# Optimization experiments

Hardware: AMD Instinct MI355X
Metric: run time of the kernel (lower is better)

## Reference

```python
import jax, jax.numpy as jnp
import numpy as np

B, N, D, C = 8, 400, 768, 3
K = 0.4
# Original keeps ranked positions whose argsort value (original index) < k*N.
# That count is static: M = #{j in [0,N) : j < k*N}
M = int(np.sum(np.arange(N) < K * N))  # 160
# static off-diagonal pair index lists (i != j), row-major like the nested loops
_ii, _jj = np.nonzero(~np.eye(M, dtype=bool))
II = jnp.asarray(_ii)
JJ = jnp.asarray(_jj)


def setup_inputs() -> dict:
    key = jax.random.key(0)
    k1, k2, k3, k4 = jax.random.split(key, 4)
    x = jax.random.normal(k1, (B, N, D), dtype=jnp.float32)
    w_span = jax.random.normal(k2, (D, 1), dtype=jnp.float32) * 0.02
    b_span = jnp.zeros((1,), dtype=jnp.float32)
    w_pair = jax.random.normal(k3, (3 * D, C), dtype=jnp.float32) * 0.02
    b_pair = jnp.zeros((C,), dtype=jnp.float32)
    span_ranges = jax.random.randint(k4, (N, 2), 0, 40, dtype=jnp.int32)
    return {"x": x, "w_span": w_span, "b_span": b_span,
            "w_pair": w_pair, "b_pair": b_pair, "span_ranges": span_ranges}


def reference(x, w_span, b_span, w_pair, b_pair, span_ranges):
    # span scorer: Linear(D,1) + sigmoid -> [B, N]
    h = jax.nn.sigmoid(x @ w_span + b_span)[..., 0]
    # torch.argsort(descending=True)
    order = jnp.argsort(-h, axis=-1)  # [B, N], original span indices in rank order
    # keep ranked positions j where order[b, j] < k*N (exactly M per row)
    pos = jnp.sort(jnp.where(order < K * N, jnp.arange(N), N), axis=-1)[:, :M]  # [B, M]
    # gather selected spans (built under no_grad in the original)
    x_ranked = jax.lax.stop_gradient(jnp.take_along_axis(x, pos[:, :, None], axis=1))  # [B, M, D]
    ranges_ranked = span_ranges[pos]  # [B, M, 2]

    # pair scorer decomposed over the concat [x_i, x_j, x_i*x_j]
    w1, w2, w3 = w_pair[:D], w_pair[D:2 * D], w_pair[2 * D:]
    a = x_ranked @ w1  # [B, M, C] contribution of x_i
    b = x_ranked @ w2  # [B, M, C] contribution of x_j
    mult = x_ranked[:, :, None, :] * x_ranked[:, None, :, :]  # [B, M, M, D]
    logits = a[:, :, None, :] + b[:, None, :, :] + mult @ w3 + b_pair  # [B, M, M, C]
    probs = jax.nn.softmax(jax.nn.sigmoid(logits), axis=-1)

    pair_probs = probs[:, II, JJ]  # [B, M*(M-1), C], off-diagonal pairs
    pair_ranges = jnp.stack([ranges_ranked[:, II], ranges_ranked[:, JJ]], axis=2)  # [B, P, 2, 2]
    return pair_probs, pair_ranges
```

## Files before the change

kernel.cpp:

```cpp
#include <hip/hip_runtime.h>
#include <math.h>

constexpr int B_ = 8;
constexpr int N_ = 400;
constexpr int D_ = 768;
constexpr int M_ = 160;
constexpr int PAIRS_ = M_ * (M_ - 1);
constexpr size_t BMD_ = (size_t)B_ * M_ * D_;

typedef __attribute__((ext_vector_type(8))) short short8;
typedef __attribute__((ext_vector_type(4))) float floatx4;


__device__ __forceinline__ short f2bf(float f) {
  unsigned u = __float_as_uint(f);
  return (short)((u + 0x7fffu + ((u >> 16) & 1u)) >> 16);
}

__global__ __launch_bounds__(256) void k_span(const float* __restrict__ x,
                                              const float* __restrict__ w_span,
                                              double* __restrict__ z) {
  int row = blockIdx.x * 4 + (threadIdx.x >> 6);
  int lane = threadIdx.x & 63;
  const float* xr = x + (size_t)row * D_;
  double acc = 0.0;
#pragma unroll
  for (int it = 0; it < 3; ++it) {
    int d = it * 256 + lane * 4;
    float4 xv = *(const float4*)(xr + d);
    float4 wv = *(const float4*)(w_span + d);
    acc += (double)xv.x * wv.x + (double)xv.y * wv.y +
           (double)xv.z * wv.z + (double)xv.w * wv.w;
  }
#pragma unroll
  for (int off = 32; off > 0; off >>= 1)
    acc += __shfl_down(acc, off, 64);
  if (lane == 0) z[row] = acc;
}

__global__ __launch_bounds__(256) void k_rank(const double* __restrict__ z,
                                              int* __restrict__ pos) {
  __shared__ double zsh[N_];
  __shared__ int ranksh[M_];
  int b = blockIdx.x;
  int t = threadIdx.x;
  for (int j = t; j < N_; j += 256) zsh[j] = z[b * N_ + j];
  __syncthreads();
  if (t < M_) {
    double zi = zsh[t];
    int cnt = 0;
    for (int j = 0; j < N_; ++j) {
      double zj = zsh[j];
      cnt += (zj > zi) || (zj == zi && j < t);
    }
    ranksh[t] = cnt;
  }
  __syncthreads();
  if (t < M_) {
    int r = ranksh[t];
    int slot = 0;
#pragma unroll 8
    for (int k = 0; k < M_; ++k) slot += (ranksh[k] < r);
    pos[b * M_ + slot] = r;
  }
}

__global__ __launch_bounds__(256) void k_prep_ranked(const float* __restrict__ x,
                                                     const float* __restrict__ w_pair,
                                                     const float* __restrict__ b_pair,
                                                     const int* __restrict__ pos,
                                                     const int* __restrict__ span_ranges,
                                                     float* __restrict__ aterm,
                                                     float* __restrict__ bterm,
                                                     int* __restrict__ rr,
                                                     short* __restrict__ Xbf,
                                                     short* __restrict__ Ybf) {
  int s = blockIdx.x * 4 + (threadIdx.x >> 6);
  int lane = threadIdx.x & 63;
  int b = s / M_;
  int row = pos[s];
  const float* xr = x + ((size_t)(b * N_ + row)) * D_;
  const float* w3 = w_pair + 2 * D_ * 3;

  float a0 = 0, a1 = 0, a2 = 0, c0 = 0, c1 = 0, c2 = 0;
#pragma unroll
  for (int it = 0; it < 3; ++it) {
    int d = it * 256 + lane * 4;
    float4 xv = *(const float4*)(xr + d);
    float xf[4] = {xv.x, xv.y, xv.z, xv.w};

    float w1v[12], w2v[12], w3v[12];
#pragma unroll
    for (int q = 0; q < 3; ++q) {
      *(float4*)(w1v + 4 * q) = *(const float4*)(w_pair + (size_t)d * 3 + 4 * q);
      *(float4*)(w2v + 4 * q) = *(const float4*)(w_pair + (size_t)(D_ + d) * 3 + 4 * q);
      *(float4*)(w3v + 4 * q) = *(const float4*)(w3 + (size_t)d * 3 + 4 * q);
    }
#pragma unroll
    for (int e = 0; e < 4; ++e) {
      a0 += xf[e] * w1v[e * 3 + 0];
      a1 += xf[e] * w1v[e * 3 + 1];
      a2 += xf[e] * w1v[e * 3 + 2];
      c0 += xf[e] * w2v[e * 3 + 0];
      c1 += xf[e] * w2v[e * 3 + 1];
      c2 += xf[e] * w2v[e * 3 + 2];
    }

    size_t o = (size_t)s * D_ + d;
    *(short4*)(Xbf + o) = make_short4(f2bf(xf[0]), f2bf(xf[1]), f2bf(xf[2]), f2bf(xf[3]));
#pragma unroll
    for (int c = 0; c < 3; ++c) {
      *(short4*)(Ybf + (size_t)c * BMD_ + o) =
          make_short4(f2bf(xf[0] * w3v[0 * 3 + c]), f2bf(xf[1] * w3v[1 * 3 + c]),
                      f2bf(xf[2] * w3v[2 * 3 + c]), f2bf(xf[3] * w3v[3 * 3 + c]));
    }
  }
#pragma unroll
  for (int off = 32; off > 0; off >>= 1) {
    a0 += __shfl_down(a0, off, 64);
    a1 += __shfl_down(a1, off, 64);
    a2 += __shfl_down(a2, off, 64);
    c0 += __shfl_down(c0, off, 64);
    c1 += __shfl_down(c1, off, 64);
    c2 += __shfl_down(c2, off, 64);
  }
  if (lane == 0) {
    aterm[s * 3 + 0] = a0 + b_pair[0];
    aterm[s * 3 + 1] = a1 + b_pair[1];
    aterm[s * 3 + 2] = a2 + b_pair[2];
    bterm[s * 3 + 0] = c0;
    bterm[s * 3 + 1] = c1;
    bterm[s * 3 + 2] = c2;
    *(int2*)(rr + s * 2) = *(const int2*)(span_ranges + row * 2);
  }
}

__global__ __launch_bounds__(256) void k_pairs(const short* __restrict__ Xbf,
                                               const short* __restrict__ Ybf,
                                               const float* __restrict__ aterm,
                                               const float* __restrict__ bterm,
                                               const int* __restrict__ rr,
                                               float* __restrict__ out_probs,
                                               float4* __restrict__ out_ranges) {
  int lane = threadIdx.x & 63;
  int w = blockIdx.x * 4 + (threadIdx.x >> 6);
  int b = w / 100;
  int t = w - b * 100;
  int ti = t / 10;
  int tj = t - ti * 10;
  int quad = lane >> 4;
  int l16 = lane & 15;

  size_t oa = ((size_t)(b * M_ + ti * 16 + l16)) * D_ + quad * 8;
  size_t ob = ((size_t)(b * M_ + tj * 16 + l16)) * D_ + quad * 8;

  const short* ah0 = Ybf + 0 * BMD_ + oa;
  const short* ah1 = Ybf + 1 * BMD_ + oa;
  const short* ah2 = Ybf + 2 * BMD_ + oa;
  const short* bhp = Xbf + ob;

  floatx4 acc0 = {0.f, 0.f, 0.f, 0.f};
  floatx4 acc1 = {0.f, 0.f, 0.f, 0.f};
  floatx4 acc2 = {0.f, 0.f, 0.f, 0.f};

#pragma unroll 6
  for (int k = 0; k < D_; k += 32) {
    short8 bh = *(const short8*)(bhp + k);
    short8 h0 = *(const short8*)(ah0 + k);
    short8 h1 = *(const short8*)(ah1 + k);
    short8 h2 = *(const short8*)(ah2 + k);
    acc0 = __builtin_amdgcn_mfma_f32_16x16x32_bf16(h0, bh, acc0, 0, 0, 0);
    acc1 = __builtin_amdgcn_mfma_f32_16x16x32_bf16(h1, bh, acc1, 0, 0, 0);
    acc2 = __builtin_amdgcn_mfma_f32_16x16x32_bf16(h2, bh, acc2, 0, 0, 0);
  }

  const float* at = aterm + (size_t)(b * M_) * 3;
  const float* bt = bterm + (size_t)(b * M_) * 3;
  const int* rrb = rr + (size_t)(b * M_) * 2;
  int j = tj * 16 + l16;
  float bj0 = bt[j * 3 + 0], bj1 = bt[j * 3 + 1], bj2 = bt[j * 3 + 2];
  int rj0 = rrb[j * 2 + 0], rj1 = rrb[j * 2 + 1];

#pragma unroll
  for (int r = 0; r < 4; ++r) {
    int i = ti * 16 + quad * 4 + r;
    if (i == j) continue;
    float l0 = acc0[r] + at[i * 3 + 0] + bj0;
    float l1 = acc1[r] + at[i * 3 + 1] + bj1;
    float l2 = acc2[r] + at[i * 3 + 2] + bj2;
    float s0 = 1.0f / (1.0f + expf(-l0));
    float s1 = 1.0f / (1.0f + expf(-l1));
    float s2 = 1.0f / (1.0f + expf(-l2));
    float e0 = expf(s0), e1 = expf(s1), e2 = expf(s2);
    float inv = 1.0f / (e0 + e1 + e2);
    int jj = j - (j > i ? 1 : 0);
    size_t p = (size_t)b * PAIRS_ + (size_t)i * (M_ - 1) + jj;
    out_probs[p * 3 + 0] = e0 * inv;
    out_probs[p * 3 + 1] = e1 * inv;
    out_probs[p * 3 + 2] = e2 * inv;
    float4 rg;
    rg.x = (float)rrb[i * 2 + 0];
    rg.y = (float)rrb[i * 2 + 1];
    rg.z = (float)rj0;
    rg.w = (float)rj1;
    out_ranges[p] = rg;
  }
}

extern "C" void kernel_launch(void* const* d_in, const int* in_sizes, int n_in,
                              void* d_out, int out_size, void* d_ws, size_t ws_size,
                              hipStream_t stream) {
  const float* x = (const float*)d_in[0];
  const float* w_span = (const float*)d_in[1];
  const float* w_pair = (const float*)d_in[3];
  const float* b_pair = (const float*)d_in[4];
  const int* span_ranges = (const int*)d_in[5];

  char* ws = (char*)d_ws;
  double* z = (double*)ws;
  int* pos = (int*)(ws + 25600);
  float* aterm = (float*)(ws + 30720);
  float* bterm = (float*)(ws + 46080);
  int* rr = (int*)(ws + 61440);
  short* Xbf = (short*)(ws + 71680);
  short* Ybf = (short*)(ws + 2037760);

  float* out = (float*)d_out;
  float* out_probs = out;
  float4* out_ranges = (float4*)(out + (size_t)B_ * PAIRS_ * 3);

  k_span<<<(B_ * N_) / 4, 256, 0, stream>>>(x, w_span, z);
  k_rank<<<B_, 256, 0, stream>>>(z, pos);
  k_prep_ranked<<<(B_ * M_) / 4, 256, 0, stream>>>(x, w_pair, b_pair, pos,
                                                   span_ranges, aterm, bterm,
                                                   rr, Xbf, Ybf);
  k_pairs<<<(B_ * 100) / 4, 256, 0, stream>>>(Xbf, Ybf, aterm, bterm, rr,
                                              out_probs, out_ranges);
}
```

Before: 106.2 us.

## Fuse span scoring with pair prep over all rows and split-K the pair MFMA

The span-score kernel now also computes the a/b projection terms and the bf16 X and X*w3 operands for all N rows, so the separate gather-and-prep kernel after ranking goes away. The pair kernel instead reads selected rows indirectly through pos. The pair kernel also splits the D reduction across four waves per block and combines their partial results through shared memory, giving four times as many waves. The cost is prep work and workspace writes for 400 rows instead of 160, plus an LDS reduction and a barrier in the pair kernel.

```diff
diff --git a/kernel.cpp b/kernel.cpp
--- a/kernel.cpp
+++ b/kernel.cpp
@@ -6,7 +6,7 @@
 constexpr int D_ = 768;
 constexpr int M_ = 160;
 constexpr int PAIRS_ = M_ * (M_ - 1);
-constexpr size_t BMD_ = (size_t)B_ * M_ * D_;
+constexpr size_t BND_ = (size_t)B_ * N_ * D_;
 
 typedef __attribute__((ext_vector_type(8))) short short8;
 typedef __attribute__((ext_vector_type(4))) float floatx4;
@@ -17,25 +17,76 @@
   return (short)((u + 0x7fffu + ((u >> 16) & 1u)) >> 16);
 }
 
-__global__ __launch_bounds__(256) void k_span(const float* __restrict__ x,
+__global__ __launch_bounds__(256) void k_prep(const float* __restrict__ x,
                                               const float* __restrict__ w_span,
-                                              double* __restrict__ z) {
+                                              const float* __restrict__ w_pair,
+                                              const float* __restrict__ b_pair,
+                                              double* __restrict__ z,
+                                              float* __restrict__ aterm,
+                                              float* __restrict__ bterm,
+                                              short* __restrict__ Xbf,
+                                              short* __restrict__ Ybf) {
   int row = blockIdx.x * 4 + (threadIdx.x >> 6);
   int lane = threadIdx.x & 63;
   const float* xr = x + (size_t)row * D_;
+  const float* w3 = w_pair + 2 * D_ * 3;
+
   double acc = 0.0;
+  float a0 = 0, a1 = 0, a2 = 0, c0 = 0, c1 = 0, c2 = 0;
 #pragma unroll
   for (int it = 0; it < 3; ++it) {
     int d = it * 256 + lane * 4;
     float4 xv = *(const float4*)(xr + d);
-    float4 wv = *(const float4*)(w_span + d);
-    acc += (double)xv.x * wv.x + (double)xv.y * wv.y +
-           (double)xv.z * wv.z + (double)xv.w * wv.w;
-  }
-#pragma unroll
-  for (int off = 32; off > 0; off >>= 1)
+    float4 sv = *(const float4*)(w_span + d);
+    acc += (double)xv.x * sv.x + (double)xv.y * sv.y +
+           (double)xv.z * sv.z + (double)xv.w * sv.w;
+    float xf[4] = {xv.x, xv.y, xv.z, xv.w};
+
+    float w1v[12], w2v[12], w3v[12];
+#pragma unroll
+    for (int q = 0; q < 3; ++q) {
+      *(float4*)(w1v + 4 * q) = *(const float4*)(w_pair + (size_t)d * 3 + 4 * q);
+      *(float4*)(w2v + 4 * q) = *(const float4*)(w_pair + (size_t)(D_ + d) * 3 + 4 * q);
+      *(float4*)(w3v + 4 * q) = *(const float4*)(w3 + (size_t)d * 3 + 4 * q);
+    }
+#pragma unroll
+    for (int e = 0; e < 4; ++e) {
+      a0 += xf[e] * w1v[e * 3 + 0];
+      a1 += xf[e] * w1v[e * 3 + 1];
+      a2 += xf[e] * w1v[e * 3 + 2];
+      c0 += xf[e] * w2v[e * 3 + 0];
+      c1 += xf[e] * w2v[e * 3 + 1];
+      c2 += xf[e] * w2v[e * 3 + 2];
+    }
+
+    size_t o = (size_t)row * D_ + d;
+    *(short4*)(Xbf + o) = make_short4(f2bf(xf[0]), f2bf(xf[1]), f2bf(xf[2]), f2bf(xf[3]));
+#pragma unroll
+    for (int c = 0; c < 3; ++c) {
+      *(short4*)(Ybf + (size_t)c * BND_ + o) =
+          make_short4(f2bf(xf[0] * w3v[0 * 3 + c]), f2bf(xf[1] * w3v[1 * 3 + c]),
+                      f2bf(xf[2] * w3v[2 * 3 + c]), f2bf(xf[3] * w3v[3 * 3 + c]));
+    }
+  }
+#pragma unroll
+  for (int off = 32; off > 0; off >>= 1) {
     acc += __shfl_down(acc, off, 64);
-  if (lane == 0) z[row] = acc;
+    a0 += __shfl_down(a0, off, 64);
+    a1 += __shfl_down(a1, off, 64);
+    a2 += __shfl_down(a2, off, 64);
+    c0 += __shfl_down(c0, off, 64);
+    c1 += __shfl_down(c1, off, 64);
+    c2 += __shfl_down(c2, off, 64);
+  }
+  if (lane == 0) {
+    z[row] = acc;
+    aterm[row * 3 + 0] = a0 + b_pair[0];
+    aterm[row * 3 + 1] = a1 + b_pair[1];
+    aterm[row * 3 + 2] = a2 + b_pair[2];
+    bterm[row * 3 + 0] = c0;
+    bterm[row * 3 + 1] = c1;
+    bterm[row * 3 + 2] = c2;
+  }
 }
 
 __global__ __launch_bounds__(256) void k_rank(const double* __restrict__ z,
@@ -65,106 +116,43 @@
   }
 }
 
-__global__ __launch_bounds__(256) void k_prep_ranked(const float* __restrict__ x,
-                                                     const float* __restrict__ w_pair,
-                                                     const float* __restrict__ b_pair,
-                                                     const int* __restrict__ pos,
-                                                     const int* __restrict__ span_ranges,
-                                                     float* __restrict__ aterm,
-                                                     float* __restrict__ bterm,
-                                                     int* __restrict__ rr,
-                                                     short* __restrict__ Xbf,
-                                                     short* __restrict__ Ybf) {
-  int s = blockIdx.x * 4 + (threadIdx.x >> 6);
-  int lane = threadIdx.x & 63;
-  int b = s / M_;
-  int row = pos[s];
-  const float* xr = x + ((size_t)(b * N_ + row)) * D_;
-  const float* w3 = w_pair + 2 * D_ * 3;
-
-  float a0 = 0, a1 = 0, a2 = 0, c0 = 0, c1 = 0, c2 = 0;
-#pragma unroll
-  for (int it = 0; it < 3; ++it) {
-    int d = it * 256 + lane * 4;
-    float4 xv = *(const float4*)(xr + d);
-    float xf[4] = {xv.x, xv.y, xv.z, xv.w};
-
-    float w1v[12], w2v[12], w3v[12];
-#pragma unroll
-    for (int q = 0; q < 3; ++q) {
-      *(float4*)(w1v + 4 * q) = *(const float4*)(w_pair + (size_t)d * 3 + 4 * q);
-      *(float4*)(w2v + 4 * q) = *(const float4*)(w_pair + (size_t)(D_ + d) * 3 + 4 * q);
-      *(float4*)(w3v + 4 * q) = *(const float4*)(w3 + (size_t)d * 3 + 4 * q);
-    }
-#pragma unroll
-    for (int e = 0; e < 4; ++e) {
-      a0 += xf[e] * w1v[e * 3 + 0];
-      a1 += xf[e] * w1v[e * 3 + 1];
-      a2 += xf[e] * w1v[e * 3 + 2];
-      c0 += xf[e] * w2v[e * 3 + 0];
-      c1 += xf[e] * w2v[e * 3 + 1];
-      c2 += xf[e] * w2v[e * 3 + 2];
-    }
-
-    size_t o = (size_t)s * D_ + d;
-    *(short4*)(Xbf + o) = make_short4(f2bf(xf[0]), f2bf(xf[1]), f2bf(xf[2]), f2bf(xf[3]));
-#pragma unroll
-    for (int c = 0; c < 3; ++c) {
-      *(short4*)(Ybf + (size_t)c * BMD_ + o) =
-          make_short4(f2bf(xf[0] * w3v[0 * 3 + c]), f2bf(xf[1] * w3v[1 * 3 + c]),
-                      f2bf(xf[2] * w3v[2 * 3 + c]), f2bf(xf[3] * w3v[3 * 3 + c]));
-    }
-  }
-#pragma unroll
-  for (int off = 32; off > 0; off >>= 1) {
-    a0 += __shfl_down(a0, off, 64);
-    a1 += __shfl_down(a1, off, 64);
-    a2 += __shfl_down(a2, off, 64);
-    c0 += __shfl_down(c0, off, 64);
-    c1 += __shfl_down(c1, off, 64);
-    c2 += __shfl_down(c2, off, 64);
-  }
-  if (lane == 0) {
-    aterm[s * 3 + 0] = a0 + b_pair[0];
-    aterm[s * 3 + 1] = a1 + b_pair[1];
-    aterm[s * 3 + 2] = a2 + b_pair[2];
-    bterm[s * 3 + 0] = c0;
-    bterm[s * 3 + 1] = c1;
-    bterm[s * 3 + 2] = c2;
-    *(int2*)(rr + s * 2) = *(const int2*)(span_ranges + row * 2);
-  }
-}
-
 __global__ __launch_bounds__(256) void k_pairs(const short* __restrict__ Xbf,
                                                const short* __restrict__ Ybf,
+                                               const int* __restrict__ pos,
                                                const float* __restrict__ aterm,
                                                const float* __restrict__ bterm,
-                                               const int* __restrict__ rr,
+                                               const int* __restrict__ span_ranges,
                                                float* __restrict__ out_probs,
                                                float4* __restrict__ out_ranges) {
+  __shared__ float red[3 * 64 * 13];
+
   int lane = threadIdx.x & 63;
-  int w = blockIdx.x * 4 + (threadIdx.x >> 6);
-  int b = w / 100;
-  int t = w - b * 100;
+  int wv = threadIdx.x >> 6;
+  int blk = blockIdx.x;
+  int b = blk / 100;
+  int t = blk - b * 100;
   int ti = t / 10;
   int tj = t - ti * 10;
   int quad = lane >> 4;
   int l16 = lane & 15;
 
-  size_t oa = ((size_t)(b * M_ + ti * 16 + l16)) * D_ + quad * 8;
-  size_t ob = ((size_t)(b * M_ + tj * 16 + l16)) * D_ + quad * 8;
-
-  const short* ah0 = Ybf + 0 * BMD_ + oa;
-  const short* ah1 = Ybf + 1 * BMD_ + oa;
-  const short* ah2 = Ybf + 2 * BMD_ + oa;
+  const int* posb = pos + b * M_;
+  int pa = posb[ti * 16 + l16];
+  int pb = posb[tj * 16 + l16];
+  size_t oa = ((size_t)(b * N_ + pa)) * D_ + wv * 192 + quad * 8;
+  size_t ob = ((size_t)(b * N_ + pb)) * D_ + wv * 192 + quad * 8;
+
+  const short* ah0 = Ybf + 0 * BND_ + oa;
+  const short* ah1 = Ybf + 1 * BND_ + oa;
+  const short* ah2 = Ybf + 2 * BND_ + oa;
   const short* bhp = Xbf + ob;
 
   floatx4 acc0 = {0.f, 0.f, 0.f, 0.f};
   floatx4 acc1 = {0.f, 0.f, 0.f, 0.f};
   floatx4 acc2 = {0.f, 0.f, 0.f, 0.f};
 
-#pragma unroll 6
-  for (int k = 0; k < D_; k += 32) {
+#pragma unroll
+  for (int k = 0; k < 192; k += 32) {
     short8 bh = *(const short8*)(bhp + k);
     short8 h0 = *(const short8*)(ah0 + k);
     short8 h1 = *(const short8*)(ah1 + k);
@@ -174,20 +162,43 @@
     acc2 = __builtin_amdgcn_mfma_f32_16x16x32_bf16(h2, bh, acc2, 0, 0, 0);
   }
 
-  const float* at = aterm + (size_t)(b * M_) * 3;
-  const float* bt = bterm + (size_t)(b * M_) * 3;
-  const int* rrb = rr + (size_t)(b * M_) * 2;
+  if (wv > 0) {
+    int base = ((wv - 1) * 64 + lane) * 13;
+#pragma unroll
+    for (int r = 0; r < 4; ++r) {
+      red[base + r] = acc0[r];
+      red[base + 4 + r] = acc1[r];
+      red[base + 8 + r] = acc2[r];
+    }
+  }
+  __syncthreads();
+  if (wv != 0) return;
+
+#pragma unroll
+  for (int u = 0; u < 3; ++u) {
+    int base = (u * 64 + lane) * 13;
+#pragma unroll
+    for (int r = 0; r < 4; ++r) {
+      acc0[r] += red[base + r];
+      acc1[r] += red[base + 4 + r];
+      acc2[r] += red[base + 8 + r];
+    }
+  }
+
+  const float* at = aterm + (size_t)(b * N_) * 3;
+  const float* bt = bterm + (size_t)(b * N_) * 3;
   int j = tj * 16 + l16;
-  float bj0 = bt[j * 3 + 0], bj1 = bt[j * 3 + 1], bj2 = bt[j * 3 + 2];
-  int rj0 = rrb[j * 2 + 0], rj1 = rrb[j * 2 + 1];
+  float bj0 = bt[pb * 3 + 0], bj1 = bt[pb * 3 + 1], bj2 = bt[pb * 3 + 2];
+  int rj0 = span_ranges[pb * 2 + 0], rj1 = span_ranges[pb * 2 + 1];
 
 #pragma unroll
   for (int r = 0; r < 4; ++r) {
     int i = ti * 16 + quad * 4 + r;
     if (i == j) continue;
-    float l0 = acc0[r] + at[i * 3 + 0] + bj0;
-    float l1 = acc1[r] + at[i * 3 + 1] + bj1;
-    float l2 = acc2[r] + at[i * 3 + 2] + bj2;
+    int pi = posb[i];
+    float l0 = acc0[r] + at[pi * 3 + 0] + bj0;
+    float l1 = acc1[r] + at[pi * 3 + 1] + bj1;
+    float l2 = acc2[r] + at[pi * 3 + 2] + bj2;
     float s0 = 1.0f / (1.0f + expf(-l0));
     float s1 = 1.0f / (1.0f + expf(-l1));
     float s2 = 1.0f / (1.0f + expf(-l2));
@@ -199,8 +210,8 @@
     out_probs[p * 3 + 1] = e1 * inv;
     out_probs[p * 3 + 2] = e2 * inv;
     float4 rg;
-    rg.x = (float)rrb[i * 2 + 0];
-    rg.y = (float)rrb[i * 2 + 1];
+    rg.x = (float)span_ranges[pi * 2 + 0];
+    rg.y = (float)span_ranges[pi * 2 + 1];
     rg.z = (float)rj0;
     rg.w = (float)rj1;
     out_ranges[p] = rg;
@@ -220,20 +231,17 @@
   double* z = (double*)ws;
   int* pos = (int*)(ws + 25600);
   float* aterm = (float*)(ws + 30720);
-  float* bterm = (float*)(ws + 46080);
-  int* rr = (int*)(ws + 61440);
-  short* Xbf = (short*)(ws + 71680);
-  short* Ybf = (short*)(ws + 2037760);
+  float* bterm = (float*)(ws + 69120);
+  short* Xbf = (short*)(ws + 107520);
+  short* Ybf = (short*)(ws + 5022720);
 
   float* out = (float*)d_out;
   float* out_probs = out;
   float4* out_ranges = (float4*)(out + (size_t)B_ * PAIRS_ * 3);
 
-  k_span<<<(B_ * N_) / 4, 256, 0, stream>>>(x, w_span, z);
+  k_prep<<<(B_ * N_) / 4, 256, 0, stream>>>(x, w_span, w_pair, b_pair, z,
+                                            aterm, bterm, Xbf, Ybf);
   k_rank<<<B_, 256, 0, stream>>>(z, pos);
-  k_prep_ranked<<<(B_ * M_) / 4, 256, 0, stream>>>(x, w_pair, b_pair, pos,
-                                                   span_ranges, aterm, bterm,
-                                                   rr, Xbf, Ybf);
-  k_pairs<<<(B_ * 100) / 4, 256, 0, stream>>>(Xbf, Ybf, aterm, bterm, rr,
-                                              out_probs, out_ranges);
-}
+  k_pairs<<<B_ * 100, 256, 0, stream>>>(Xbf, Ybf, pos, aterm, bterm,
+                                        span_ranges, out_probs, out_ranges);
+}
```

Measured after the change: 107.4 us. About the same (+1.1%).
